# Kernel optimization log

Hardware: AMD Instinct MI355X
Metric: run time of the kernel (lower is better)

The kernel has to match this reference:

```python
import jax, jax.numpy as jnp
import numpy as np

WS = (5, 8, 8)   # window_size (Wz, Wh, Ww)
SS = (2, 4, 4)   # shift_size  (Sz, Sh, Sw)
EPS = 1e-5


def _rel_pos_index(ws):
    Wz, Wh, Ww = ws
    coords = np.stack(np.meshgrid(np.arange(Wz), np.arange(Wh), np.arange(Ww), indexing='ij'))
    cf = coords.reshape(3, -1)                      # (3, N)
    rel = cf[:, :, None] - cf[:, None, :]           # (3, N, N)
    rel = rel.transpose(1, 2, 0).astype(np.int64)   # (N, N, 3)
    rel[..., 0] += Wz - 1
    rel[..., 1] += Wh - 1
    rel[..., 2] += Ww - 1
    rel[..., 0] *= (2 * Wh - 1) * (2 * Ww - 1)
    rel[..., 1] *= (2 * Ww - 1)
    return rel.sum(-1)                              # (N, N)


def _shift_mask(Z, H, W, ws, ss):
    Wz, Wh, Ww = ws
    Sz, Sh, Sw = ss
    img = np.zeros((Z, H, W), dtype=np.float32)
    cnt = 0
    for zs in (slice(0, -Wz), slice(-Wz, -Sz), slice(-Sz, None)):
        for hs in (slice(0, -Wh), slice(-Wh, -Sh), slice(-Sh, None)):
            for wl in (slice(0, -Ww), slice(-Ww, -Sw), slice(-Sw, None)):
                img[zs, hs, wl] = cnt
                cnt += 1
    mw = img.reshape(Z // Wz, Wz, H // Wh, Wh, W // Ww, Ww)
    mw = mw.transpose(0, 2, 4, 1, 3, 5).reshape(-1, Wz * Wh * Ww)  # (nW, N)
    diff = mw[:, None, :] - mw[:, :, None]                          # (nW, N, N)
    return np.where(diff != 0, np.float32(-100.0), np.float32(0.0))


def _layernorm(x, g, b):
    mu = jnp.mean(x, axis=-1, keepdims=True)
    var = jnp.var(x, axis=-1, keepdims=True)
    return (x - mu) * jax.lax.rsqrt(var + EPS) * g + b


def setup_inputs() -> dict:
    key = jax.random.key(0)
    ks = jax.random.split(key, 6)
    B, C, Z, H, W = 2, 192, 10, 48, 48
    nH = 6
    hidden = 4 * C
    tbl = (2 * WS[0] - 1) * (2 * WS[1] - 1) * (2 * WS[2] - 1)
    return {
        'x': jax.random.normal(ks[0], (B, C, Z, H, W), jnp.float32),
        'norm1_g': jnp.ones((C,), jnp.float32),
        'norm1_b': jnp.zeros((C,), jnp.float32),
        'qkv_w': jax.random.normal(ks[1], (3 * C, C), jnp.float32) * 0.02,
        'qkv_b': jnp.zeros((3 * C,), jnp.float32),
        'proj_w': jax.random.normal(ks[2], (C, C), jnp.float32) * 0.02,
        'proj_b': jnp.zeros((C,), jnp.float32),
        'rpb_table': jax.random.normal(ks[3], (tbl, nH), jnp.float32) * 0.02,
        'norm2_g': jnp.ones((C,), jnp.float32),
        'norm2_b': jnp.zeros((C,), jnp.float32),
        'fc1_w': jax.random.normal(ks[4], (hidden, C), jnp.float32) * 0.02,
        'fc1_b': jnp.zeros((hidden,), jnp.float32),
        'fc2_w': jax.random.normal(ks[5], (C, hidden), jnp.float32) * 0.02,
        'fc2_b': jnp.zeros((C,), jnp.float32),
    }


def reference(x, norm1_g, norm1_b, qkv_w, qkv_b, proj_w, proj_b, rpb_table,
              norm2_g, norm2_b, fc1_w, fc1_b, fc2_w, fc2_b):
    B, C, Z, H, W = x.shape
    Wz, Wh, Ww = WS
    Sz, Sh, Sw = SS
    nH = rpb_table.shape[1]
    hd = C // nH
    N = Wz * Wh * Ww
    scale = hd ** -0.5

    h = jnp.transpose(x, (0, 2, 3, 4, 1))            # (B,Z,H,W,C) channels-last
    shortcut = h
    h = _layernorm(h, norm1_g, norm1_b)
    # cyclic shift
    h = jnp.roll(h, shift=(-Sz, -Sh, -Sw), axis=(1, 2, 3))
    # window partition -> (BW, N, C)
    win = h.reshape(B, Z // Wz, Wz, H // Wh, Wh, W // Ww, Ww, C)
    win = win.transpose(0, 1, 3, 5, 2, 4, 6, 7).reshape(-1, N, C)
    BW = win.shape[0]

    qkv = win @ qkv_w.T + qkv_b                      # (BW, N, 3C)
    qkv = qkv.reshape(BW, N, 3, nH, hd)
    q = jnp.transpose(qkv[:, :, 0], (0, 2, 1, 3)) * scale   # (BW,nH,N,hd)
    k = jnp.transpose(qkv[:, :, 1], (0, 2, 1, 3))
    v = jnp.transpose(qkv[:, :, 2], (0, 2, 1, 3))

    attn = jnp.einsum('bhnd,bhmd->bhnm', q, k)       # (BW,nH,N,N)
    idx = _rel_pos_index(WS)                          # static (N,N)
    bias = rpb_table[idx.reshape(-1)].reshape(N, N, nH)
    attn = attn + jnp.transpose(bias, (2, 0, 1))[None]

    mask = jnp.asarray(_shift_mask(Z, H, W, WS, SS)) # (nW,N,N), static
    nW = mask.shape[0]
    attn = attn.reshape(B, nW, nH, N, N) + mask[None, :, None]
    attn = jax.nn.softmax(attn.reshape(BW, nH, N, N), axis=-1)

    out = jnp.einsum('bhnm,bhmd->bhnd', attn, v)     # (BW,nH,N,hd)
    out = jnp.transpose(out, (0, 2, 1, 3)).reshape(BW, N, C)
    out = out @ proj_w.T + proj_b

    # window reverse -> (B,Z,H,W,C)
    out = out.reshape(B, Z // Wz, H // Wh, W // Ww, Wz, Wh, Ww, C)
    out = out.transpose(0, 1, 4, 2, 5, 3, 6, 7).reshape(B, Z, H, W, C)
    out = jnp.roll(out, shift=(Sz, Sh, Sw), axis=(1, 2, 3))

    h = shortcut + out
    h2 = _layernorm(h, norm2_g, norm2_b)
    h2 = jax.nn.gelu(h2 @ fc1_w.T + fc1_b, approximate=False)
    h2 = h2 @ fc2_w.T + fc2_b
    h = h + h2
    return jnp.transpose(h, (0, 4, 1, 2, 3))          # back to (B,C,Z,H,W)
```

## Files before the change

### kernel.cpp

```cpp
#include <hip/hip_runtime.h>
#include <hip/hip_bf16.h>

typedef __hip_bfloat16 bf16;
typedef __attribute__((ext_vector_type(4))) float f32x4;
typedef __attribute__((ext_vector_type(8))) short bf16x8;
typedef __attribute__((ext_vector_type(4))) short bf16x4;
typedef __attribute__((ext_vector_type(4))) int i32x4;

#define DEVINL __device__ __forceinline__

constexpr int SPB = 23040;
constexpr int TOK = 46080;
constexpr int NWT = 320;
constexpr int NHEAD = 6;
constexpr int HD = 32;
constexpr int HID = 768;
constexpr int TBL = 2025;
constexpr float SCALE = 0.17677669529663687f;

DEVINL float b2f(bf16 v) { return __bfloat162float(v); }
DEVINL float bflo(unsigned u) { unsigned w = u << 16; return __builtin_bit_cast(float, w); }

DEVINL unsigned cvtpk(float a, float b) {
  unsigned r;
  asm("v_cvt_pk_bf16_f32 %0, %1, %2" : "=v"(r) : "v"(a), "v"(b));
  return r;
}

DEVINL f32x4 mfma16(bf16x4 a, bf16x4 b, f32x4 c) {
#if __has_builtin(__builtin_amdgcn_mfma_f32_16x16x16bf16_1k)
  return __builtin_amdgcn_mfma_f32_16x16x16bf16_1k(a, b, c, 0, 0, 0);
#elif __has_builtin(__builtin_amdgcn_mfma_f32_16x16x16_bf16)
  return __builtin_amdgcn_mfma_f32_16x16x16_bf16(a, b, c, 0, 0, 0);
#else
  f32x4 d;
  asm volatile("v_mfma_f32_16x16x16_bf16 %0, %1, %2, %3\n\ts_nop 7\n\ts_nop 7"
               : "=v"(d) : "v"(a), "v"(b), "v"(c));
  return d;
#endif
}

DEVINL void gload16(const bf16* g, bf16* l) {
  __builtin_amdgcn_global_load_lds(
      (const __attribute__((address_space(1))) void*)g,
      (__attribute__((address_space(3))) void*)l, 16, 0, 0);
}

__global__ void k_flag(const unsigned* __restrict__ g1, int* __restrict__ flag) {
  if (threadIdx.x == 0) flag[0] = (g1[0] == 0x3F800000u) ? 1 : 0;
}

struct CvtArgs {
  const void* src[13];
  bf16* dst[13];
  int n[13];
};

__global__ __launch_bounds__(256) void k_cvt(CvtArgs a, const int* __restrict__ flag) {
  int bi = blockIdx.y;
  int n = a.n[bi];
  bool f32m = flag[0] != 0;
  const float* sf = (const float*)a.src[bi];
  const bf16* sh = (const bf16*)a.src[bi];
  bf16* d = a.dst[bi];
  if (f32m) {
    for (int i = blockIdx.x * 256 + threadIdx.x; i < n; i += gridDim.x * 256)
      d[i] = __float2bfloat16(sf[i]);
  } else {
    for (int i = blockIdx.x * 256 + threadIdx.x; i < n; i += gridDim.x * 256)
      d[i] = sh[i];
  }
}

__global__ __launch_bounds__(256) void k_ln1win(
    const void* __restrict__ xv, const bf16* __restrict__ g, const bf16* __restrict__ be,
    const int* __restrict__ flag, float* __restrict__ hbuf, bf16* __restrict__ win) {
  __shared__ float tile[192][64];
  __shared__ float red[2][4][64];
  __shared__ float stat[2][64];
  int t = threadIdx.x;
  int p = t & 63, q = t >> 6;
  int base = blockIdx.x * 64;
  int b = base / SPB, s0 = base % SPB;
  bool f32m = flag[0] != 0;
  float sum = 0.f, sq = 0.f;
  if (f32m) {
    const float* x = (const float*)xv;
    for (int c = q; c < 192; c += 4) {
      float v = x[(long)(b * 192 + c) * SPB + s0 + p];
      tile[c][p] = v; sum += v; sq += v * v;
    }
  } else {
    const bf16* x = (const bf16*)xv;
    for (int c = q; c < 192; c += 4) {
      float v = b2f(x[(long)(b * 192 + c) * SPB + s0 + p]);
      tile[c][p] = v; sum += v; sq += v * v;
    }
  }
  red[0][q][p] = sum; red[1][q][p] = sq;
  __syncthreads();
  if (t < 64) {
    float s1 = red[0][0][t] + red[0][1][t] + red[0][2][t] + red[0][3][t];
    float s2 = red[1][0][t] + red[1][1][t] + red[1][2][t] + red[1][3][t];
    float mu = s1 * (1.f / 192.f);
    float var = s2 * (1.f / 192.f) - mu * mu;
    stat[0][t] = mu;
    stat[1][t] = rsqrtf(var + 1e-5f);
  }
  __syncthreads();
  int p2 = t >> 2, quad = t & 3;
  int spos = s0 + p2;
  int z = spos / 2304, rm = spos % 2304;
  int hh = rm / 48, ww = rm % 48;
  int zr = z - 2; if (zr < 0) zr += 10;
  int hr = hh - 4; if (hr < 0) hr += 48;
  int wr = ww - 4; if (wr < 0) wr += 48;
  int zw = zr / 5, zi = zr - zw * 5;
  int hw = hr >> 3, hi = hr & 7;
  int wv = wr >> 3, wi = wr & 7;
  int wb = ((b * 2 + zw) * 6 + hw) * 6 + wv;
  int n = (zi * 8 + hi) * 8 + wi;
  float mu = stat[0][p2], rs = stat[1][p2];
  long hb = (long)(b * SPB + spos) * 192;
  long wbse = (long)(wb * NWT + n) * 192;
  for (int c = quad * 48; c < quad * 48 + 48; ++c) {
    float v = tile[c][p2];
    hbuf[hb + c] = v;
    win[wbse + c] = __float2bfloat16((v - mu) * rs * b2f(g[c]) + b2f(be[c]));
  }
}

template <int EPI, int NN>
__global__ __launch_bounds__(256, 5) void k_gemm(
    const bf16* __restrict__ A, const bf16* __restrict__ Wt, const bf16* __restrict__ bias,
    int K, bf16* __restrict__ out0, float* __restrict__ hbuf, void* __restrict__ outb,
    const int* __restrict__ flag) {
  __shared__ __align__(16) char smem[24576];
  bf16* As = (bf16*)smem;
  bf16* Bs = (bf16*)(smem + 16384);

  int t = threadIdx.x;
  constexpr int NBLK = 360 * NN;
  int wg = (blockIdx.x & 7) * (NBLK / 8) + (blockIdx.x >> 3);
  int m0 = (wg / NN) * 128, n0 = (wg % NN) * 64;
  int wave = t >> 6, lane = t & 63;
  int lr = lane & 15, lg = lane >> 4;
  int wbase = t & ~63;
  f32x4 acc[2][4];
#pragma unroll
  for (int a = 0; a < 2; ++a)
#pragma unroll
    for (int bb2 = 0; bb2 < 4; ++bb2) acc[a][bb2] = (f32x4){0.f, 0.f, 0.f, 0.f};

  for (int kc = 0; kc < K; kc += 64) {
#pragma unroll
    for (int it = 0; it < 4; ++it) {
      int s = it * 256 + t;
      int r = s >> 3, c = s & 7;
      int cg = c ^ (r & 7);
      gload16(&A[(long)(m0 + r) * K + kc + cg * 8], As + (it * 256 + wbase) * 8);
    }
#pragma unroll
    for (int it = 0; it < 2; ++it) {
      int s = it * 256 + t;
      int r = s >> 3, c = s & 7;
      int cg = c ^ (r & 7);
      gload16(&Wt[(long)(n0 + r) * K + kc + cg * 8], Bs + (it * 256 + wbase) * 8);
    }
    __syncthreads();
#pragma unroll
    for (int ks = 0; ks < 2; ++ks) {
      int ra = wave * 32 + lr;
      bf16x8 a0 = *(const bf16x8*)(As + ra * 64 + (((ks * 4 + lg) ^ (ra & 7)) * 8));
      bf16x8 a1 = *(const bf16x8*)(As + (ra + 16) * 64 + (((ks * 4 + lg) ^ ((ra + 16) & 7)) * 8));
#pragma unroll
      for (int nn = 0; nn < 4; ++nn) {
        int rb = nn * 16 + lr;
        bf16x8 bfr = *(const bf16x8*)(Bs + rb * 64 + (((ks * 4 + lg) ^ (rb & 7)) * 8));
        acc[0][nn] = __builtin_amdgcn_mfma_f32_16x16x32_bf16(a0, bfr, acc[0][nn], 0, 0, 0);
        acc[1][nn] = __builtin_amdgcn_mfma_f32_16x16x32_bf16(a1, bfr, acc[1][nn], 0, 0, 0);
      }
    }
    __syncthreads();
  }

  if constexpr (EPI == 0) {
    bf16* Ct = (bf16*)smem;
#pragma unroll
    for (int nn = 0; nn < 4; ++nn) {
      int f = n0 + nn * 16 + lr;
      float bv = b2f(bias[f]);
      float sc = (f < 192) ? SCALE : 1.f;
#pragma unroll
      for (int mi = 0; mi < 2; ++mi)
#pragma unroll
        for (int r = 0; r < 4; ++r) {
          int rl = wave * 32 + mi * 16 + lg * 4 + r;
          Ct[rl * 72 + nn * 16 + lr] = __float2bfloat16((acc[mi][nn][r] + bv) * sc);
        }
    }
    __syncthreads();
#pragma unroll
    for (int it = 0; it < 4; ++it) {
      int fi = it * 256 + t;
      int row = fi >> 3, c8 = (fi & 7) * 8;
      int f0 = n0 + c8;
      int plane = f0 >> 5, d0 = f0 & 31;
      long dst = ((long)plane * TOK + m0 + row) * 32 + d0;
      *(i32x4*)&out0[dst] = *(const i32x4*)&Ct[row * 72 + c8];
    }
  } else if constexpr (EPI == 2) {
    bf16* Ct = (bf16*)smem;
#pragma unroll
    for (int nn = 0; nn < 4; ++nn) {
      int f = n0 + nn * 16 + lr;
      float bv = b2f(bias[f]);
#pragma unroll
      for (int mi = 0; mi < 2; ++mi)
#pragma unroll
        for (int r = 0; r < 4; ++r) {
          int rl = wave * 32 + mi * 16 + lg * 4 + r;
          float v = acc[mi][nn][r] + bv;
          v = 0.5f * v * (1.f + erff(v * 0.70710678118654752f));
          Ct[rl * 72 + nn * 16 + lr] = __float2bfloat16(v);
        }
    }
    __syncthreads();
#pragma unroll
    for (int it = 0; it < 4; ++it) {
      int fi = it * 256 + t;
      int row = fi >> 3, c8 = (fi & 7) * 8;
      long dst = (long)(m0 + row) * HID + n0 + c8;
      *(i32x4*)&out0[dst] = *(const i32x4*)&Ct[row * 72 + c8];
    }
  } else {
    float* eld = (float*)smem;
    int b = m0 / SPB, sbase = m0 % SPB;
    bool f32m = flag[0] != 0;
#pragma unroll
    for (int half = 0; half < 2; ++half) {
      if ((wave >> 1) == half) {
#pragma unroll
        for (int nn = 0; nn < 4; ++nn) {
          int c = n0 + nn * 16 + lr;
          float bv = b2f(bias[c]);
#pragma unroll
          for (int mi = 0; mi < 2; ++mi)
#pragma unroll
            for (int r = 0; r < 4; ++r) {
              int rl = wave * 32 + mi * 16 + lg * 4 + r;
              int row = m0 + rl;
              float v = acc[mi][nn][r] + bv + hbuf[(long)row * 192 + c];
              eld[(rl - half * 64) * 65 + nn * 16 + lr] = v;
            }
        }
      }
      __syncthreads();
      int cl = t >> 2, sq = t & 3;
      long ob = (long)(b * 192 + n0 + cl) * SPB + sbase + half * 64;
      if (f32m) {
        float* ob32 = (float*)outb;
#pragma unroll
        for (int k2 = 0; k2 < 16; ++k2) {
          int sl = sq * 16 + k2;
          ob32[ob + sl] = eld[sl * 65 + cl];
        }
      } else {
        bf16* ob16 = (bf16*)outb;
#pragma unroll
        for (int k2 = 0; k2 < 16; ++k2) {
          int sl = sq * 16 + k2;
          ob16[ob + sl] = __float2bfloat16(eld[sl * 65 + cl]);
        }
      }
      __syncthreads();
    }
  }
}

__global__ __launch_bounds__(256) void k_projln2(
    const bf16* __restrict__ A, const bf16* __restrict__ Wt, const bf16* __restrict__ bias,
    const bf16* __restrict__ g2, const bf16* __restrict__ b2,
    float* __restrict__ hbuf, bf16* __restrict__ lnout) {
  __shared__ __align__(16) char smem[32768];
  bf16* As = (bf16*)smem;
  bf16* Bs = (bf16*)(smem + 8192);

  int t = threadIdx.x;
  int wg = (blockIdx.x & 7) * 90 + (blockIdx.x >> 3);
  int m0 = wg * 64;
  int wave = t >> 6, lane = t & 63;
  int lr = lane & 15, lg = lane >> 4;
  int wbase = t & ~63;
  f32x4 acc[12];
#pragma unroll
  for (int bb2 = 0; bb2 < 12; ++bb2) acc[bb2] = (f32x4){0.f, 0.f, 0.f, 0.f};

  for (int kc = 0; kc < 192; kc += 64) {
#pragma unroll
    for (int it = 0; it < 2; ++it) {
      int s = it * 256 + t;
      int r = s >> 3, c = s & 7;
      int cg = c ^ (r & 7);
      gload16(&A[(long)(m0 + r) * 192 + kc + cg * 8], As + (it * 256 + wbase) * 8);
    }
#pragma unroll
    for (int it = 0; it < 6; ++it) {
      int s = it * 256 + t;
      int r = s >> 3, c = s & 7;
      int cg = c ^ (r & 7);
      gload16(&Wt[(long)r * 192 + kc + cg * 8], Bs + (it * 256 + wbase) * 8);
    }
    __syncthreads();
#pragma unroll
    for (int ks = 0; ks < 2; ++ks) {
      int ra = wave * 16 + lr;
      bf16x8 a0 = *(const bf16x8*)(As + ra * 64 + (((ks * 4 + lg) ^ (ra & 7)) * 8));
#pragma unroll
      for (int nn = 0; nn < 12; ++nn) {
        int rb = nn * 16 + lr;
        bf16x8 bfr = *(const bf16x8*)(Bs + rb * 64 + (((ks * 4 + lg) ^ (rb & 7)) * 8));
        acc[nn] = __builtin_amdgcn_mfma_f32_16x16x32_bf16(a0, bfr, acc[nn], 0, 0, 0);
      }
    }
    __syncthreads();
  }

#pragma unroll
  for (int r = 0; r < 4; ++r) {
    int grow = m0 + wave * 16 + lg * 4 + r;
    int wb = grow / NWT, i = grow % NWT;
    int b = wb / 72, wIdx = wb % 72;
    int zw = wIdx / 36, hw = (wIdx % 36) / 6, wv = wIdx % 6;
    int zi = i >> 6, hi = (i >> 3) & 7, wi = i & 7;
    int zf = zw * 5 + zi + 2; if (zf >= 10) zf -= 10;
    int hf = hw * 8 + hi + 4; if (hf >= 48) hf -= 48;
    int wf = wv * 8 + wi + 4; if (wf >= 48) wf -= 48;
    long s = (long)(b * SPB + zf * 2304 + hf * 48 + wf);
    float v[12];
    float sum = 0.f, sq = 0.f;
#pragma unroll
    for (int nn = 0; nn < 12; ++nn) {
      int c = nn * 16 + lr;
      float x = acc[nn][r] + b2f(bias[c]) + hbuf[s * 192 + c];
      v[nn] = x;
      hbuf[s * 192 + c] = x;
      sum += x;
      sq += x * x;
    }
#pragma unroll
    for (int off = 1; off < 16; off <<= 1) {
      sum += __shfl_xor(sum, off);
      sq += __shfl_xor(sq, off);
    }
    float mu = sum * (1.f / 192.f);
    float rs = rsqrtf(sq * (1.f / 192.f) - mu * mu + 1e-5f);
#pragma unroll
    for (int nn = 0; nn < 12; ++nn) {
      int c = nn * 16 + lr;
      lnout[s * 192 + c] = __float2bfloat16((v[nn] - mu) * rs * b2f(g2[c]) + b2f(b2[c]));
    }
  }
}

__global__ __launch_bounds__(256) void k_attn_mfma(
    const bf16* __restrict__ qkv, const bf16* __restrict__ rpb, bf16* __restrict__ o) {
  __shared__ __align__(16) bf16 KlA[320 * 32];
  __shared__ __align__(16) bf16 Vt[32][328];
  __shared__ unsigned short bias_l[2032];
  __shared__ unsigned short info[320];

  int t = threadIdx.x;
  int blk = blockIdx.x;
  int head = blk % NHEAD, wb = blk / NHEAD;
  const bf16* qp = qkv + ((long)head * TOK + wb * NWT) * HD;
  const bf16* kp = qkv + ((long)(6 + head) * TOK + wb * NWT) * HD;
  const bf16* vp = qkv + ((long)(12 + head) * TOK + wb * NWT) * HD;
  int wIdx = wb % 72;
  int wz = wIdx / 36, hw = (wIdx % 36) / 6, wv = wIdx % 6;
  int wbase = t & ~63;

#pragma unroll
  for (int it = 0; it < 5; ++it) {
    int s = it * 256 + t;
    int row = s >> 2, c = s & 3;
    int cg = c ^ (row & 3);
    gload16(&kp[row * 32 + cg * 8], KlA + (it * 256 + wbase) * 8);
  }
#pragma unroll
  for (int it = 0; it < 3; ++it) {
    int idx = t + 256 * it;
    if (idx < 640) {
      int kp2 = idx % 160, c8 = idx / 160;
      i32x4 va = *(const i32x4*)&vp[(kp2 * 2) * HD + c8 * 8];
      i32x4 vb = *(const i32x4*)&vp[(kp2 * 2 + 1) * HD + c8 * 8];
#pragma unroll
      for (int e = 0; e < 8; ++e) {
        unsigned lo = ((unsigned)va[e >> 1] >> ((e & 1) * 16)) & 0xffffu;
        unsigned hi = ((unsigned)vb[e >> 1] >> ((e & 1) * 16)) & 0xffffu;
        *(unsigned*)&Vt[c8 * 8 + e][kp2 * 2] = lo | (hi << 16);
      }
    }
  }
  for (int idx = t; idx < TBL; idx += 256)
    bias_l[idx] = ((const unsigned short*)rpb)[idx * NHEAD + head];
  for (int idx = t; idx < NWT; idx += 256) {
    int zi = idx >> 6, hi2 = (idx >> 3) & 7, wi = idx & 7;
    int zr = wz * 5 + zi, hr = hw * 8 + hi2, wr = wv * 8 + wi;
    int rid = (zr < 5 ? 0 : (zr < 8 ? 9 : 18)) + (hr < 40 ? 0 : (hr < 44 ? 3 : 6)) +
              (wr < 40 ? 0 : (wr < 44 ? 1 : 2));
    info[idx] = (unsigned short)(((zi * 225 + hi2 * 15 + wi) << 5) | rid);
  }
  __syncthreads();

  int wave = t >> 6, lane = t & 63;
  int lr = lane & 15, lg = lane >> 4;
  int csw = (lg ^ (lr & 3)) * 8;

  for (int qi = 0; qi < 5; ++qi) {
    int qbl = qi * 64 + wave * 16;
    bf16x8 qf = *(const bf16x8*)&qp[(qbl + lr) * HD + lg * 8];
    unsigned ciq = info[qbl + lr];
    int ci1012 = (int)(ciq >> 5) + 1012;

    float mph0, sph0, mph1, sph1;
    f32x4 oa00, oa01, oa10, oa11;

#pragma unroll
    for (int ph = 0; ph < 2; ++ph) {
      f32x4 sc[10];
#pragma unroll
      for (int u = 0; u < 10; ++u) {
        int tt = ph * 10 + u;
        bf16x8 kf = *(const bf16x8*)(KlA + (tt * 16 + lr) * 32 + csw);
        sc[u] = __builtin_amdgcn_mfma_f32_16x16x32_bf16(kf, qf, (f32x4){0.f, 0.f, 0.f, 0.f}, 0, 0, 0);
      }
      float mxv = -1e30f;
#pragma unroll
      for (int u = 0; u < 10; ++u) {
        int tt = ph * 10 + u;
        int k0 = tt * 16 + lg * 4;
        unsigned w0 = *(const unsigned*)&info[k0];
        unsigned w1 = *(const unsigned*)&info[k0 + 2];
        unsigned kin0 = w0 & 0xffffu, kin1 = w0 >> 16;
        unsigned kin2 = w1 & 0xffffu, kin3 = w1 >> 16;
        float s0 = sc[u][0] + bflo((unsigned)bias_l[ci1012 - (int)(kin0 >> 5)]);
        float s1 = sc[u][1] + bflo((unsigned)bias_l[ci1012 - (int)(kin1 >> 5)]);
        float s2 = sc[u][2] + bflo((unsigned)bias_l[ci1012 - (int)(kin2 >> 5)]);
        float s3 = sc[u][3] + bflo((unsigned)bias_l[ci1012 - (int)(kin3 >> 5)]);
        if ((kin0 ^ ciq) & 31u) s0 -= 100.f;
        if ((kin1 ^ ciq) & 31u) s1 -= 100.f;
        if ((kin2 ^ ciq) & 31u) s2 -= 100.f;
        if ((kin3 ^ ciq) & 31u) s3 -= 100.f;
        sc[u][0] = s0; sc[u][1] = s1; sc[u][2] = s2; sc[u][3] = s3;
        mxv = fmaxf(mxv, fmaxf(fmaxf(s0, s1), fmaxf(s2, s3)));
      }
      mxv = fmaxf(mxv, __shfl_xor(mxv, 16));
      mxv = fmaxf(mxv, __shfl_xor(mxv, 32));
      float sum = 0.f;
#pragma unroll
      for (int u = 0; u < 10; ++u) {
        float p0 = __expf(sc[u][0] - mxv);
        float p1 = __expf(sc[u][1] - mxv);
        float p2 = __expf(sc[u][2] - mxv);
        float p3 = __expf(sc[u][3] - mxv);
        sc[u][0] = p0; sc[u][1] = p1; sc[u][2] = p2; sc[u][3] = p3;
        sum += (p0 + p1) + (p2 + p3);
      }
      sum += __shfl_xor(sum, 16);
      sum += __shfl_xor(sum, 32);

      f32x4 o0 = {0.f, 0.f, 0.f, 0.f}, o1 = {0.f, 0.f, 0.f, 0.f};
#pragma unroll
      for (int u = 0; u < 10; ++u) {
        int tt = ph * 10 + u;
        unsigned pk0 = cvtpk(sc[u][0], sc[u][1]);
        unsigned pk1 = cvtpk(sc[u][2], sc[u][3]);
        union { unsigned uu[2]; bf16x4 v; } pu;
        pu.uu[0] = pk0; pu.uu[1] = pk1;
        bf16x4 v0 = *(const bf16x4*)&Vt[lr][tt * 16 + lg * 4];
        bf16x4 v1 = *(const bf16x4*)&Vt[16 + lr][tt * 16 + lg * 4];
        o0 = mfma16(pu.v, v0, o0);
        o1 = mfma16(pu.v, v1, o1);
      }
      if (ph == 0) { mph0 = mxv; sph0 = sum; oa00 = o0; oa01 = o1; }
      else         { mph1 = mxv; sph1 = sum; oa10 = o0; oa11 = o1; }
    }

    float m = fmaxf(mph0, mph1);
    float f0 = __expf(mph0 - m), f1 = __expf(mph1 - m);
    float rl = 1.f / (sph0 * f0 + sph1 * f1);
    float a0 = f0 * rl, a1 = f1 * rl;
    int a0i = __builtin_bit_cast(int, a0);
    int a1i = __builtin_bit_cast(int, a1);
#pragma unroll
    for (int r = 0; r < 4; ++r) {
      float s0 = __builtin_bit_cast(float, __builtin_amdgcn_ds_bpermute((lg * 4 + r) * 4, a0i));
      float s1 = __builtin_bit_cast(float, __builtin_amdgcn_ds_bpermute((lg * 4 + r) * 4, a1i));
      bf16* pr = o + ((long)(wb * NWT) + qbl + lg * 4 + r) * 192 + head * 32;
      pr[lr] = __float2bfloat16(oa00[r] * s0 + oa10[r] * s1);
      pr[16 + lr] = __float2bfloat16(oa01[r] * s0 + oa11[r] * s1);
    }
  }
}

extern "C" void kernel_launch(void* const* d_in, const int* in_sizes, int n_in,
                              void* d_out, int out_size, void* d_ws, size_t ws_size,
                              hipStream_t stream) {
  (void)in_sizes; (void)n_in; (void)out_size; (void)ws_size;

  char* pp = (char*)d_ws;
  float* hbuf = (float*)pp;        pp += (size_t)TOK * 192 * 4;
  bf16* qkv   = (bf16*)pp;         pp += (size_t)3 * TOK * 192 * 2;
  bf16* win   = (bf16*)pp;         pp += (size_t)TOK * 192 * 2;
  bf16* fc1o  = (bf16*)pp;         pp += (size_t)TOK * HID * 2;
  int*  flag  = (int*)pp;          pp += 64;

  bf16* ln2o = qkv;

  const int din_idx[13] = {1, 2, 3, 4, 5, 6, 7, 8, 9, 10, 11, 12, 13};
  const int sizes[13]   = {192, 192, 110592, 576, 36864, 192, 12150, 192, 192,
                           147456, 768, 147456, 192};
  bf16* canon[13];
  for (int ii = 0; ii < 13; ++ii) {
    canon[ii] = (bf16*)pp;
    size_t bytes = ((size_t)sizes[ii] * 2 + 63) & ~(size_t)63;
    pp += bytes;
  }
  bf16* n1g  = canon[0];
  bf16* n1b  = canon[1];
  bf16* qkvw = canon[2];
  bf16* qkvb = canon[3];
  bf16* projw= canon[4];
  bf16* projb= canon[5];
  bf16* rpb  = canon[6];
  bf16* n2g  = canon[7];
  bf16* n2b  = canon[8];
  bf16* fc1w = canon[9];
  bf16* fc1b = canon[10];
  bf16* fc2w = canon[11];
  bf16* fc2b = canon[12];

  CvtArgs ca;
  for (int ii = 0; ii < 13; ++ii) {
    ca.src[ii] = d_in[din_idx[ii]];
    ca.dst[ii] = canon[ii];
    ca.n[ii] = sizes[ii];
  }

  k_flag<<<1, 64, 0, stream>>>((const unsigned*)d_in[1], flag);
  k_cvt<<<dim3(64, 13), 256, 0, stream>>>(ca, flag);
  k_ln1win<<<TOK / 64, 256, 0, stream>>>(d_in[0], n1g, n1b, flag, hbuf, win);
  k_gemm<0, 9><<<360 * 9, 256, 0, stream>>>(win, qkvw, qkvb, 192, qkv, nullptr, nullptr, flag);
  k_attn_mfma<<<864, 256, 0, stream>>>(qkv, rpb, win);
  k_projln2<<<720, 256, 0, stream>>>(win, projw, projb, n2g, n2b, hbuf, ln2o);
  k_gemm<2, 12><<<360 * 12, 256, 0, stream>>>(ln2o, fc1w, fc1b, 192, fc1o, nullptr, nullptr, flag);
  k_gemm<3, 3><<<360 * 3, 256, 0, stream>>>(fc1o, fc2w, fc2b, 768, nullptr, hbuf, d_out, flag);
}
```

Before: 227.9 us.

## Retile FC1 and FC2 GEMMs into dedicated 64x192 tile kernels

Replaces the generic templated GEMM for the MLP layers with two specialized kernels that each compute a 64-row by 192-column output tile per block, with waves splitting rows instead of columns. FC2 now produces all 192 output channels per block, so the A tile of the 768-wide hidden activations is loaded once rather than three times. FC1 splits the 768 outputs into four 192-wide tiles. The aim is more A-tile reuse and fewer blocks, at the cost of 12 accumulators per wave and a larger epilogue staging buffer.

```diff
diff --git a/kernel.cpp b/kernel.cpp
--- a/kernel.cpp
+++ b/kernel.cpp
@@ -209,72 +209,6 @@
       long dst = ((long)plane * TOK + m0 + row) * 32 + d0;
       *(i32x4*)&out0[dst] = *(const i32x4*)&Ct[row * 72 + c8];
     }
-  } else if constexpr (EPI == 2) {
-    bf16* Ct = (bf16*)smem;
-#pragma unroll
-    for (int nn = 0; nn < 4; ++nn) {
-      int f = n0 + nn * 16 + lr;
-      float bv = b2f(bias[f]);
-#pragma unroll
-      for (int mi = 0; mi < 2; ++mi)
-#pragma unroll
-        for (int r = 0; r < 4; ++r) {
-          int rl = wave * 32 + mi * 16 + lg * 4 + r;
-          float v = acc[mi][nn][r] + bv;
-          v = 0.5f * v * (1.f + erff(v * 0.70710678118654752f));
-          Ct[rl * 72 + nn * 16 + lr] = __float2bfloat16(v);
-        }
-    }
-    __syncthreads();
-#pragma unroll
-    for (int it = 0; it < 4; ++it) {
-      int fi = it * 256 + t;
-      int row = fi >> 3, c8 = (fi & 7) * 8;
-      long dst = (long)(m0 + row) * HID + n0 + c8;
-      *(i32x4*)&out0[dst] = *(const i32x4*)&Ct[row * 72 + c8];
-    }
-  } else {
-    float* eld = (float*)smem;
-    int b = m0 / SPB, sbase = m0 % SPB;
-    bool f32m = flag[0] != 0;
-#pragma unroll
-    for (int half = 0; half < 2; ++half) {
-      if ((wave >> 1) == half) {
-#pragma unroll
-        for (int nn = 0; nn < 4; ++nn) {
-          int c = n0 + nn * 16 + lr;
-          float bv = b2f(bias[c]);
-#pragma unroll
-          for (int mi = 0; mi < 2; ++mi)
-#pragma unroll
-            for (int r = 0; r < 4; ++r) {
-              int rl = wave * 32 + mi * 16 + lg * 4 + r;
-              int row = m0 + rl;
-              float v = acc[mi][nn][r] + bv + hbuf[(long)row * 192 + c];
-              eld[(rl - half * 64) * 65 + nn * 16 + lr] = v;
-            }
-        }
-      }
-      __syncthreads();
-      int cl = t >> 2, sq = t & 3;
-      long ob = (long)(b * 192 + n0 + cl) * SPB + sbase + half * 64;
-      if (f32m) {
-        float* ob32 = (float*)outb;
-#pragma unroll
-        for (int k2 = 0; k2 < 16; ++k2) {
-          int sl = sq * 16 + k2;
-          ob32[ob + sl] = eld[sl * 65 + cl];
-        }
-      } else {
-        bf16* ob16 = (bf16*)outb;
-#pragma unroll
-        for (int k2 = 0; k2 < 16; ++k2) {
-          int sl = sq * 16 + k2;
-          ob16[ob + sl] = __float2bfloat16(eld[sl * 65 + cl]);
-        }
-      }
-      __syncthreads();
-    }
   }
 }
 
@@ -360,6 +294,164 @@
       int c = nn * 16 + lr;
       lnout[s * 192 + c] = __float2bfloat16((v[nn] - mu) * rs * b2f(g2[c]) + b2f(b2[c]));
     }
+  }
+}
+
+__global__ __launch_bounds__(256) void k_fc1(
+    const bf16* __restrict__ A, const bf16* __restrict__ Wt, const bf16* __restrict__ bias,
+    bf16* __restrict__ out) {
+  __shared__ __align__(16) char smem[32768];
+  bf16* As = (bf16*)smem;
+  bf16* Bs = (bf16*)(smem + 8192);
+
+  int t = threadIdx.x;
+  int wg = (blockIdx.x & 7) * 360 + (blockIdx.x >> 3);
+  int nt = wg & 3;
+  int m0 = (wg >> 2) * 64;
+  int wave = t >> 6, lane = t & 63;
+  int lr = lane & 15, lg = lane >> 4;
+  int wbase = t & ~63;
+  f32x4 acc[12];
+#pragma unroll
+  for (int bb2 = 0; bb2 < 12; ++bb2) acc[bb2] = (f32x4){0.f, 0.f, 0.f, 0.f};
+
+  for (int kc = 0; kc < 192; kc += 64) {
+#pragma unroll
+    for (int it = 0; it < 2; ++it) {
+      int s = it * 256 + t;
+      int r = s >> 3, c = s & 7;
+      int cg = c ^ (r & 7);
+      gload16(&A[(long)(m0 + r) * 192 + kc + cg * 8], As + (it * 256 + wbase) * 8);
+    }
+#pragma unroll
+    for (int it = 0; it < 6; ++it) {
+      int s = it * 256 + t;
+      int r = s >> 3, c = s & 7;
+      int cg = c ^ (r & 7);
+      gload16(&Wt[(long)(nt * 192 + r) * 192 + kc + cg * 8], Bs + (it * 256 + wbase) * 8);
+    }
+    __syncthreads();
+#pragma unroll
+    for (int ks = 0; ks < 2; ++ks) {
+      int ra = wave * 16 + lr;
+      bf16x8 a0 = *(const bf16x8*)(As + ra * 64 + (((ks * 4 + lg) ^ (ra & 7)) * 8));
+#pragma unroll
+      for (int nn = 0; nn < 12; ++nn) {
+        int rb = nn * 16 + lr;
+        bf16x8 bfr = *(const bf16x8*)(Bs + rb * 64 + (((ks * 4 + lg) ^ (rb & 7)) * 8));
+        acc[nn] = __builtin_amdgcn_mfma_f32_16x16x32_bf16(a0, bfr, acc[nn], 0, 0, 0);
+      }
+    }
+    __syncthreads();
+  }
+
+  bf16* Ct = (bf16*)smem;
+#pragma unroll
+  for (int nn = 0; nn < 12; ++nn) {
+    int f = nt * 192 + nn * 16 + lr;
+    float bv = b2f(bias[f]);
+#pragma unroll
+    for (int r = 0; r < 4; ++r) {
+      int rl = wave * 16 + lg * 4 + r;
+      float v = acc[nn][r] + bv;
+      v = 0.5f * v * (1.f + erff(v * 0.70710678118654752f));
+      Ct[rl * 200 + nn * 16 + lr] = __float2bfloat16(v);
+    }
+  }
+  __syncthreads();
+#pragma unroll
+  for (int it = 0; it < 6; ++it) {
+    int fi = it * 256 + t;
+    int row = fi / 24, c8 = fi % 24;
+    long dst = (long)(m0 + row) * HID + nt * 192 + c8 * 8;
+    *(i32x4*)&out[dst] = *(const i32x4*)&Ct[row * 200 + c8 * 8];
+  }
+}
+
+__global__ __launch_bounds__(256) void k_fc2(
+    const bf16* __restrict__ A, const bf16* __restrict__ Wt, const bf16* __restrict__ bias,
+    const float* __restrict__ hbuf, void* __restrict__ outb, const int* __restrict__ flag) {
+  __shared__ __align__(16) char smem[32768];
+  bf16* As = (bf16*)smem;
+  bf16* Bs = (bf16*)(smem + 8192);
+
+  int t = threadIdx.x;
+  int wg = (blockIdx.x & 7) * 90 + (blockIdx.x >> 3);
+  int m0 = wg * 64;
+  int wave = t >> 6, lane = t & 63;
+  int lr = lane & 15, lg = lane >> 4;
+  int wbase = t & ~63;
+  f32x4 acc[12];
+#pragma unroll
+  for (int bb2 = 0; bb2 < 12; ++bb2) acc[bb2] = (f32x4){0.f, 0.f, 0.f, 0.f};
+
+  for (int kc = 0; kc < 768; kc += 64) {
+#pragma unroll
+    for (int it = 0; it < 2; ++it) {
+      int s = it * 256 + t;
+      int r = s >> 3, c = s & 7;
+      int cg = c ^ (r & 7);
+      gload16(&A[(long)(m0 + r) * 768 + kc + cg * 8], As + (it * 256 + wbase) * 8);
+    }
+#pragma unroll
+    for (int it = 0; it < 6; ++it) {
+      int s = it * 256 + t;
+      int r = s >> 3, c = s & 7;
+      int cg = c ^ (r & 7);
+      gload16(&Wt[(long)r * 768 + kc + cg * 8], Bs + (it * 256 + wbase) * 8);
+    }
+    __syncthreads();
+#pragma unroll
+    for (int ks = 0; ks < 2; ++ks) {
+      int ra = wave * 16 + lr;
+      bf16x8 a0 = *(const bf16x8*)(As + ra * 64 + (((ks * 4 + lg) ^ (ra & 7)) * 8));
+#pragma unroll
+      for (int nn = 0; nn < 12; ++nn) {
+        int rb = nn * 16 + lr;
+        bf16x8 bfr = *(const bf16x8*)(Bs + rb * 64 + (((ks * 4 + lg) ^ (rb & 7)) * 8));
+        acc[nn] = __builtin_amdgcn_mfma_f32_16x16x32_bf16(a0, bfr, acc[nn], 0, 0, 0);
+      }
+    }
+    __syncthreads();
+  }
+
+  float* eld = (float*)smem;
+  int b = m0 / SPB, sbase = m0 % SPB;
+  bool f32m = flag[0] != 0;
+#pragma unroll
+  for (int cc = 0; cc < 3; ++cc) {
+#pragma unroll
+    for (int nn2 = 0; nn2 < 4; ++nn2) {
+      int nn = cc * 4 + nn2;
+      int c = nn * 16 + lr;
+      float bv = b2f(bias[c]);
+#pragma unroll
+      for (int r = 0; r < 4; ++r) {
+        int rl = wave * 16 + lg * 4 + r;
+        long s = m0 + rl;
+        float x = acc[nn][r] + bv + hbuf[s * 192 + c];
+        eld[rl * 65 + nn2 * 16 + lr] = x;
+      }
+    }
+    __syncthreads();
+    int cl = t >> 2, sq = t & 3;
+    long ob = (long)(b * 192 + cc * 64 + cl) * SPB + sbase;
+    if (f32m) {
+      float* ob32 = (float*)outb;
+#pragma unroll
+      for (int k2 = 0; k2 < 16; ++k2) {
+        int sl = sq * 16 + k2;
+        ob32[ob + sl] = eld[sl * 65 + cl];
+      }
+    } else {
+      bf16* ob16 = (bf16*)outb;
+#pragma unroll
+      for (int k2 = 0; k2 < 16; ++k2) {
+        int sl = sq * 16 + k2;
+        ob16[ob + sl] = __float2bfloat16(eld[sl * 65 + cl]);
+      }
+    }
+    __syncthreads();
   }
 }
 
@@ -554,6 +646,6 @@
   k_gemm<0, 9><<<360 * 9, 256, 0, stream>>>(win, qkvw, qkvb, 192, qkv, nullptr, nullptr, flag);
   k_attn_mfma<<<864, 256, 0, stream>>>(qkv, rpb, win);
   k_projln2<<<720, 256, 0, stream>>>(win, projw, projb, n2g, n2b, hbuf, ln2o);
-  k_gemm<2, 12><<<360 * 12, 256, 0, stream>>>(ln2o, fc1w, fc1b, 192, fc1o, nullptr, nullptr, flag);
-  k_gemm<3, 3><<<360 * 3, 256, 0, stream>>>(fc1o, fc2w, fc2b, 768, nullptr, hbuf, d_out, flag);
-}
+  k_fc1<<<2880, 256, 0, stream>>>(ln2o, fc1w, fc1b, fc1o);
+  k_fc2<<<720, 256, 0, stream>>>(fc1o, fc2w, fc2b, hbuf, d_out, flag);
+}
```

After: 227.9 us. About the same (+0.0%).
